# Kernel optimization log

Measured on AMD Instinct MI355X. Metric: run time of the kernel, lower is better.

The kernel has to match this reference:

```python
import jax, jax.numpy as jnp
import numpy as np

B, C, L = 4, 512, 4096
LN_EPS = 1e-5


def setup_inputs() -> dict:
    key = jax.random.key(0)
    ks = jax.random.split(key, 6)
    s = 1.0 / np.sqrt(C)
    return {
        "x": jax.random.normal(ks[0], (B, C, L), dtype=jnp.float32),
        "ln_w": jnp.ones((C,), dtype=jnp.float32),
        "ln_b": jnp.zeros((C,), dtype=jnp.float32),
        "wq": jax.random.normal(ks[1], (C, C), dtype=jnp.float32) * s,
        "bq": jnp.zeros((C,), dtype=jnp.float32),
        "wk": jax.random.normal(ks[2], (C, C), dtype=jnp.float32) * s,
        "bk": jnp.zeros((C,), dtype=jnp.float32),
        "wv": jax.random.normal(ks[3], (C, C), dtype=jnp.float32) * s,
        "bv": jnp.zeros((C,), dtype=jnp.float32),
        "wp": jax.random.normal(ks[4], (C, C), dtype=jnp.float32) * s,
        "bp": jnp.zeros((C,), dtype=jnp.float32),
    }


def reference(x, ln_w, ln_b, wq, bq, wk, bk, wv, bv, wp, bp):
    # x: [b, c, l]. LayerNorm over channels (permute -> LN -> permute back).
    xt = jnp.swapaxes(x, 1, 2)  # [b, l, c]
    mu = jnp.mean(xt, axis=-1, keepdims=True)
    var = jnp.var(xt, axis=-1, keepdims=True)
    h = (xt - mu) * jax.lax.rsqrt(var + LN_EPS) * ln_w + ln_b  # [b, l, c]

    # 1x1 convs == channel-mixing matmuls (weight [out, in])
    q = jnp.einsum('blc,oc->blo', h, wq) + bq  # [b, l, c]
    k = jnp.einsum('blc,oc->blo', h, wk) + bk
    v = jnp.einsum('blc,oc->blo', h, wv) + bv

    c = x.shape[1]
    scores = jnp.einsum('blc,bmc->blm', q, k) * (float(c) ** -0.5)  # [b, l_q, l_k]
    attn = jax.nn.softmax(scores, axis=-1)
    o = jnp.einsum('blm,bmc->blc', attn, v)  # [b, l, c]

    o = jnp.einsum('blc,oc->blo', o, wp) + bp
    o = jax.nn.selu(o)
    return x + jnp.swapaxes(o, 1, 2)  # [b, c, l]
```

## Files before the change

### kernel.cpp

```cpp
#include <hip/hip_runtime.h>


typedef __attribute__((ext_vector_type(8))) __bf16 bf16x8;
typedef __attribute__((ext_vector_type(4))) __bf16 bf16x4;
typedef __attribute__((ext_vector_type(4))) float  f32x4;

__device__ __forceinline__ f32x4 mfma16(bf16x8 a, bf16x8 b, f32x4 c) {
  return __builtin_amdgcn_mfma_f32_16x16x32_bf16(a, b, c, 0, 0, 0);
}

__device__ __forceinline__ void gll16(const void* g, void* l) {
  __builtin_amdgcn_global_load_lds(
      (const __attribute__((address_space(1))) unsigned int*)g,
      (__attribute__((address_space(3))) unsigned int*)l, 16, 0, 0);
}

__device__ __forceinline__ float selu_f(float v) {
  return 1.0507009873554805f * (v > 0.f ? v : 1.6732632423543772f * (__expf(v) - 1.f));
}

#define QSCALE ((float)(1.4426950408889634 / 22.627416997969522))

__global__ __launch_bounds__(256) void cvt_w(const float* __restrict__ w0,
                                             const float* __restrict__ w1,
                                             const float* __restrict__ w2,
                                             const float* __restrict__ w3,
                                             __bf16* __restrict__ dst) {
  int idx = blockIdx.x * 256 + threadIdx.x;
  int which = idx >> 16;
  const float* s = which == 0 ? w0 : which == 1 ? w1 : which == 2 ? w2 : w3;
  f32x4 v = *(const f32x4*)(s + (size_t)(idx & 65535) * 4);
  bf16x4 o = {(__bf16)v.x, (__bf16)v.y, (__bf16)v.z, (__bf16)v.w};
  *(bf16x4*)(dst + (size_t)idx * 4) = o;
}

__global__ __launch_bounds__(256) void ln_stats(const float* __restrict__ x,
                                                float* __restrict__ mu,
                                                float* __restrict__ rs) {
  __shared__ float shs[4][64], shq[4][64];
  int b = blockIdx.y, l0 = blockIdx.x * 64;
  int i = threadIdx.x & 63, j = threadIdx.x >> 6;
  const float* xp = x + (size_t)b * 512 * 4096 + l0 + i;
  float s = 0.f, sq = 0.f;
  for (int c = j; c < 512; c += 4) {
    float v = xp[(size_t)c * 4096];
    s += v; sq += v * v;
  }
  shs[j][i] = s; shq[j][i] = sq;
  __syncthreads();
  if (threadIdx.x < 64) {
    float S = shs[0][i] + shs[1][i] + shs[2][i] + shs[3][i];
    float Q = shq[0][i] + shq[1][i] + shq[2][i] + shq[3][i];
    float m = S * (1.f / 512.f);
    float var = Q * (1.f / 512.f) - m * m;
    int idx = b * 4096 + l0 + i;
    mu[idx] = m;
    rs[idx] = rsqrtf(var + 1e-5f);
  }
}

__global__ __launch_bounds__(256) void ln_apply(const float* __restrict__ x,
                                                const float* __restrict__ mu,
                                                const float* __restrict__ rs,
                                                const float* __restrict__ lw,
                                                const float* __restrict__ lb,
                                                __bf16* __restrict__ h) {
  __shared__ float t[64][65];
  int b = blockIdx.z, c0 = blockIdx.y * 64, l0 = blockIdx.x * 64;
  int li = threadIdx.x & 63, r4 = threadIdx.x >> 6;
  const float* xp = x + (size_t)(b * 512 + c0) * 4096 + l0;
#pragma unroll
  for (int rr = 0; rr < 16; ++rr) {
    int cl = rr * 4 + r4;
    t[cl][li] = xp[(size_t)cl * 4096 + li];
  }
  __syncthreads();
  float gw = lw[c0 + li], gb = lb[c0 + li];
#pragma unroll
  for (int rr = 0; rr < 16; ++rr) {
    int lr = rr * 4 + r4;
    int l = l0 + lr;
    float m = mu[b * 4096 + l], r = rs[b * 4096 + l];
    float v = (t[li][lr] - m) * r * gw + gb;
    h[((size_t)b * 4096 + l) * 512 + c0 + li] = (__bf16)v;
  }
}

__global__ __launch_bounds__(256, 2) void gemm_qkv(
    const __bf16* __restrict__ A, const __bf16* __restrict__ W,
    const float* __restrict__ b0, const float* __restrict__ b1,
    const float* __restrict__ b2, __bf16* __restrict__ out,
    __bf16* __restrict__ vt) {
  __shared__ __align__(16) __bf16 As[128 * 64];
  __shared__ __align__(16) __bf16 Bs[128 * 64];
  const int tid = threadIdx.x;
  const int w = tid >> 6, lane = tid & 63, g = lane >> 4, li = lane & 15;
  const int id = blockIdx.x;
  const int jj = id >> 3;
  const int m0 = (16 * (id & 7) + jj / 12) * 128;
  const int n0 = (jj % 12) * 128;
  const int wm = w >> 1, wn = w & 1;
  const int srow = lane >> 3;
  const int scol = ((lane & 7) ^ srow) * 8;
  f32x4 acc[4][4] = {};
  for (int kt = 0; kt < 8; ++kt) {
    __syncthreads();
#pragma unroll
    for (int qq = 0; qq < 4; ++qq) {
      int r = w * 32 + qq * 8;
      gll16(A + (size_t)(m0 + r + srow) * 512 + kt * 64 + scol, &As[r * 64]);
      gll16(W + (size_t)(n0 + r + srow) * 512 + kt * 64 + scol, &Bs[r * 64]);
    }
    __syncthreads();
#pragma unroll
    for (int kk = 0; kk < 2; ++kk) {
      bf16x8 af[4], bf[4];
#pragma unroll
      for (int t = 0; t < 4; ++t) {
        int ra = wm * 64 + t * 16 + li;
        af[t] = *(const bf16x8*)&As[ra * 64 + ((kk * 32 + 8 * g) ^ ((ra & 7) * 8))];
        int rb = wn * 64 + t * 16 + li;
        bf[t] = *(const bf16x8*)&Bs[rb * 64 + ((kk * 32 + 8 * g) ^ ((rb & 7) * 8))];
      }
#pragma unroll
      for (int i = 0; i < 4; ++i)
#pragma unroll
        for (int j = 0; j < 4; ++j) acc[i][j] = mfma16(af[i], bf[j], acc[i][j]);
    }
  }
  const int which = n0 >> 9;
  if (which < 2) {
    const float* bb = which == 0 ? b0 : b1;
    const float sc = which == 0 ? QSCALE : 1.0f;
    __bf16* o = out + (size_t)which * 8388608;
#pragma unroll
    for (int i = 0; i < 4; ++i) {
#pragma unroll
      for (int j = 0; j < 4; ++j) {
        int r = m0 + wm * 64 + i * 16 + 4 * g;
        int c = (n0 & 511) + wn * 64 + j * 16 + li;
        float bv = bb[c];
#pragma unroll
        for (int e = 0; e < 4; ++e)
          o[(size_t)(r + e) * 512 + c] = (__bf16)((acc[i][j][e] + bv) * sc);
      }
    }
  } else {
#pragma unroll
    for (int i = 0; i < 4; ++i) {
#pragma unroll
      for (int j = 0; j < 4; ++j) {
        int r = m0 + wm * 64 + i * 16 + 4 * g;
        int c = (n0 & 511) + wn * 64 + j * 16 + li;
        float bv = b2[c];
#pragma unroll
        for (int e = 0; e < 4; ++e) {
          int row = r + e;
          vt[((size_t)(row >> 12) * 512 + c) * 4096 + (row & 4095)] =
              (__bf16)(acc[i][j][e] + bv);
        }
      }
    }
  }
}

__global__ __launch_bounds__(256, 2) void gemm_pp(
    const __bf16* __restrict__ A, const __bf16* __restrict__ Bm,
    const float* __restrict__ bias, const float* __restrict__ xres,
    float* __restrict__ out) {
  __shared__ __align__(16) __bf16 As[128 * 64];
  __shared__ __align__(16) __bf16 Bs[128 * 64];
  const int tid = threadIdx.x;
  const int w = tid >> 6, lane = tid & 63, g = lane >> 4, li = lane & 15;
  const int id = blockIdx.x;
  const int jj = id >> 3;
  const int n0 = (16 * (id & 7) + (jj & 15)) * 128;
  const int m0 = (jj >> 4) * 128;
  const int wm = w >> 1, wn = w & 1;
  const int srow = lane >> 3;
  const int scol = ((lane & 7) ^ srow) * 8;
  f32x4 acc[4][4] = {};
  for (int kt = 0; kt < 8; ++kt) {
    __syncthreads();
#pragma unroll
    for (int qq = 0; qq < 4; ++qq) {
      int r = w * 32 + qq * 8;
      gll16(A + (size_t)(m0 + r + srow) * 512 + kt * 64 + scol, &As[r * 64]);
      gll16(Bm + (size_t)(n0 + r + srow) * 512 + kt * 64 + scol, &Bs[r * 64]);
    }
    __syncthreads();
#pragma unroll
    for (int kk = 0; kk < 2; ++kk) {
      bf16x8 af[4], bf[4];
#pragma unroll
      for (int t = 0; t < 4; ++t) {
        int ra = wm * 64 + t * 16 + li;
        af[t] = *(const bf16x8*)&As[ra * 64 + ((kk * 32 + 8 * g) ^ ((ra & 7) * 8))];
        int rb = wn * 64 + t * 16 + li;
        bf[t] = *(const bf16x8*)&Bs[rb * 64 + ((kk * 32 + 8 * g) ^ ((rb & 7) * 8))];
      }
#pragma unroll
      for (int i = 0; i < 4; ++i)
#pragma unroll
        for (int j = 0; j < 4; ++j) acc[i][j] = mfma16(af[i], bf[j], acc[i][j]);
    }
  }
#pragma unroll
  for (int i = 0; i < 4; ++i) {
#pragma unroll
    for (int j = 0; j < 4; ++j) {
      int r = m0 + wm * 64 + i * 16 + 4 * g;
      int c = n0 + wn * 64 + j * 16 + li;
      int bb = c >> 12, l = c & 4095;
#pragma unroll
      for (int e = 0; e < 4; ++e) {
        float v = acc[i][j][e] + bias[r + e];
        size_t oi = ((size_t)bb * 512 + (r + e)) * 4096 + l;
        out[oi] = xres[oi] + selu_f(v);
      }
    }
  }
}

__global__ __launch_bounds__(512, 2) void flash_half(
    const __bf16* __restrict__ Q, const __bf16* __restrict__ K,
    const __bf16* __restrict__ VT, __bf16* __restrict__ Op,
    float* __restrict__ stats) {
  __shared__ __align__(16) __bf16 Ks[64][512];
  __shared__ __align__(16) __bf16 VTs[512][64];
  __shared__ __align__(16) __bf16 Ps[128][64];

  const int tid = threadIdx.x;
  const int w = tid >> 6, lane = tid & 63, g = lane >> 4, li = lane & 15;
  const int id = blockIdx.x;
  const int grp = id & 7;
  const int b = grp >> 1, half = grp & 1;
  const int q0 = (id >> 3) * 128;
  const size_t base = (size_t)b * (4096 * 512);
  const int kvbase = half * 2048;

  bf16x8 qf[16];
  {
    const __bf16* qp = Q + base + (size_t)(q0 + 16 * w + li) * 512 + 8 * g;
#pragma unroll
    for (int ks = 0; ks < 16; ++ks) qf[ks] = *(const bf16x8*)(qp + ks * 32);
  }

  f32x4 acc[8][4] = {};
  f32x4 lacc = {};
  bf16x8 ones;
#pragma unroll
  for (int j = 0; j < 8; ++j) ones[j] = (__bf16)1.0f;

  auto stageK = [&](int kt) {
#pragma unroll
    for (int i = 0; i < 8; ++i) {
      int r = w * 8 + i;
      int y = (lane * 16) ^ ((r & 7) << 4);
      gll16(K + base + (size_t)(kvbase + kt * 64 + r) * 512 + (y >> 1),
            &Ks[r][0]);
    }
  };
  auto stageVT = [&](int kt) {
    const int drow = lane >> 3;
    const int gr = (lane & 7) ^ drow;
#pragma unroll
    for (int i = 0; i < 8; ++i) {
      int d0 = w * 64 + i * 8;
      gll16(VT + (size_t)b * 2097152 + (size_t)(d0 + drow) * 4096 +
                kvbase + kt * 64 + gr * 8,
            &VTs[d0][0]);
    }
  };

  stageK(0);
  stageVT(0);
  __syncthreads();

  for (int kt = 0; kt < 32; ++kt) {
    __builtin_amdgcn_s_setprio(1);
    f32x4 s[4] = {};
#pragma unroll
    for (int ks = 0; ks < 16; ++ks) {
      int e = (ks * 32 + 8 * g) ^ ((li & 7) * 8);
#pragma unroll
      for (int kvt = 0; kvt < 4; ++kvt) {
        bf16x8 kf = *(const bf16x8*)&Ks[kvt * 16 + li][e];
        s[kvt] = mfma16(qf[ks], kf, s[kvt]);
      }
    }
    __builtin_amdgcn_s_setprio(0);

#pragma unroll
    for (int kvt = 0; kvt < 4; ++kvt) {
#pragma unroll
      for (int e = 0; e < 4; ++e) {
        float p = exp2f(s[kvt][e]);
        int row = 16 * w + 4 * g + e;
        int slot = (2 * kvt + (li >> 3)) ^ (row & 7);
        Ps[row][slot * 8 + (li & 7)] = (__bf16)p;
      }
    }
    __syncthreads();

    if (kt + 1 < 32) stageK(kt + 1);

#pragma unroll
    for (int ks = 0; ks < 2; ++ks) {
      bf16x8 bfr[4];
#pragma unroll
      for (int ct = 0; ct < 4; ++ct) {
        int dcol = 64 * w + 16 * ct + li;
        int slot = (4 * ks + g) ^ (li & 7);
        bfr[ct] = *(const bf16x8*)&VTs[dcol][slot * 8];
      }
      __builtin_amdgcn_s_setprio(1);
#pragma unroll
      for (int rt = 0; rt < 8; ++rt) {
        int prow = rt * 16 + li;
        int slot = (4 * ks + g) ^ (li & 7);
        bf16x8 af = *(const bf16x8*)&Ps[prow][slot * 8];
        if (rt == w) lacc = mfma16(af, ones, lacc);
#pragma unroll
        for (int ct = 0; ct < 4; ++ct)
          acc[rt][ct] = mfma16(af, bfr[ct], acc[rt][ct]);
      }
      __builtin_amdgcn_s_setprio(0);
    }
    __syncthreads();

    if (kt + 1 < 32) stageVT(kt + 1);
  }

  if (li == 0)
    *(f32x4*)(stats + half * 16384 + b * 4096 + q0 + 16 * w + 4 * g) = lacc;
#pragma unroll
  for (int rt = 0; rt < 8; ++rt) {
#pragma unroll
    for (int ct = 0; ct < 4; ++ct) {
      int rr = q0 + rt * 16 + 4 * g;
      int cc = w * 64 + ct * 16 + li;
#pragma unroll
      for (int e = 0; e < 4; ++e)
        Op[(size_t)half * 8388608 + base + (size_t)(rr + e) * 512 + cc] =
            (__bf16)acc[rt][ct][e];
    }
  }
}

__global__ __launch_bounds__(256) void combine2(const __bf16* __restrict__ Op,
                                                const float* __restrict__ stats,
                                                __bf16* __restrict__ ao) {
  int gid = blockIdx.x * 256 + threadIdx.x;
  int row = gid >> 6;
  int c = (gid & 63) * 8;
  float l0 = stats[row], l1 = stats[16384 + row];
  float inv = 1.f / (l0 + l1);
  bf16x8 v0 = *(const bf16x8*)(Op + (size_t)row * 512 + c);
  bf16x8 v1 = *(const bf16x8*)(Op + 8388608 + (size_t)row * 512 + c);
  bf16x8 o;
#pragma unroll
  for (int j = 0; j < 8; ++j)
    o[j] = (__bf16)(((float)v0[j] + (float)v1[j]) * inv);
  *(bf16x8*)(ao + (size_t)row * 512 + c) = o;
}

extern "C" void kernel_launch(void* const* d_in, const int* in_sizes, int n_in,
                              void* d_out, int out_size, void* d_ws, size_t ws_size,
                              hipStream_t stream) {
  const float* x   = (const float*)d_in[0];
  const float* lnw = (const float*)d_in[1];
  const float* lnb = (const float*)d_in[2];
  const float* wq  = (const float*)d_in[3];
  const float* bq  = (const float*)d_in[4];
  const float* wk  = (const float*)d_in[5];
  const float* bk  = (const float*)d_in[6];
  const float* wv  = (const float*)d_in[7];
  const float* bv  = (const float*)d_in[8];
  const float* wp  = (const float*)d_in[9];
  const float* bp  = (const float*)d_in[10];

  char* ws = (char*)d_ws;
  const size_t MB = 1024 * 1024;
  __bf16* h    = (__bf16*)(ws);
  __bf16* q    = (__bf16*)(ws + 16 * MB);
  __bf16* vt   = (__bf16*)(ws + 48 * MB);
  __bf16* wbf  = (__bf16*)(ws + 64 * MB);
  float*  mu   = (float*)(ws + 66 * MB);
  float*  rsg  = (float*)(ws + 66 * MB + 65536);
  __bf16* op   = (__bf16*)(ws + 67 * MB);
  float*  stats= (float*)(ws + 99 * MB);
  __bf16* ao   = h;

  cvt_w<<<1024, 256, 0, stream>>>(wq, wk, wv, wp, wbf);
  ln_stats<<<dim3(64, 4), 256, 0, stream>>>(x, mu, rsg);
  ln_apply<<<dim3(64, 8, 4), 256, 0, stream>>>(x, mu, rsg, lnw, lnb, h);
  gemm_qkv<<<1536, 256, 0, stream>>>(h, wbf, bq, bk, bv, q, vt);
  flash_half<<<256, 512, 0, stream>>>(q, q + 8388608, vt, op, stats);
  combine2<<<4096, 256, 0, stream>>>(op, stats, ao);
  gemm_pp<<<512, 256, 0, stream>>>(wbf + 3 * 262144, ao, bp, x,
                                   (float*)d_out);
}
```

Before: 341.6 us.

## Split attention KV into four partitions with smaller KV tiles

Attention now splits the key/value range into four partitions instead of two, with 32-key tiles instead of 64. This doubles the block count so every CU gets work and shrinks shared memory per block. Partial outputs go into reused scratch buffers (the LayerNorm buffer, the output buffer, a new region), and a four-way combine normalizes them. The cost is more partial-output traffic, more synchronization per key processed, and a tighter launch bound that may force register spills.

```diff
diff --git a/kernel.cpp b/kernel.cpp
--- a/kernel.cpp
+++ b/kernel.cpp
@@ -222,22 +222,25 @@
   }
 }
 
-__global__ __launch_bounds__(512, 2) void flash_half(
+__global__ __launch_bounds__(512, 4) void flash_quarter(
     const __bf16* __restrict__ Q, const __bf16* __restrict__ K,
-    const __bf16* __restrict__ VT, __bf16* __restrict__ Op,
+    const __bf16* __restrict__ VT,
+    __bf16* __restrict__ o0, __bf16* __restrict__ o1,
+    __bf16* __restrict__ o2, __bf16* __restrict__ o3,
     float* __restrict__ stats) {
-  __shared__ __align__(16) __bf16 Ks[64][512];
-  __shared__ __align__(16) __bf16 VTs[512][64];
-  __shared__ __align__(16) __bf16 Ps[128][64];
+  __shared__ __align__(16) __bf16 Ks[32][512];
+  __shared__ __align__(16) __bf16 VTs[512][32];
+  __shared__ __align__(16) __bf16 Ps[128][32];
 
   const int tid = threadIdx.x;
   const int w = tid >> 6, lane = tid & 63, g = lane >> 4, li = lane & 15;
   const int id = blockIdx.x;
-  const int grp = id & 7;
-  const int b = grp >> 1, half = grp & 1;
-  const int q0 = (id >> 3) * 128;
+  const int grp = id & 15;
+  const int b = grp >> 2, quarter = grp & 3;
+  const int q0 = (id >> 4) * 128;
   const size_t base = (size_t)b * (4096 * 512);
-  const int kvbase = half * 2048;
+  const int kvbase = quarter * 1024;
+  __bf16* Op = quarter == 0 ? o0 : quarter == 1 ? o1 : quarter == 2 ? o2 : o3;
 
   bf16x8 qf[16];
   {
@@ -254,21 +257,21 @@
 
   auto stageK = [&](int kt) {
 #pragma unroll
-    for (int i = 0; i < 8; ++i) {
-      int r = w * 8 + i;
+    for (int i = 0; i < 4; ++i) {
+      int r = w * 4 + i;
       int y = (lane * 16) ^ ((r & 7) << 4);
-      gll16(K + base + (size_t)(kvbase + kt * 64 + r) * 512 + (y >> 1),
+      gll16(K + base + (size_t)(kvbase + kt * 32 + r) * 512 + (y >> 1),
             &Ks[r][0]);
     }
   };
   auto stageVT = [&](int kt) {
-    const int drow = lane >> 3;
-    const int gr = (lane & 7) ^ drow;
-#pragma unroll
-    for (int i = 0; i < 8; ++i) {
-      int d0 = w * 64 + i * 8;
+    const int drow = lane >> 2;
+    const int gr = (lane & 3) ^ (drow & 3);
+#pragma unroll
+    for (int i = 0; i < 4; ++i) {
+      int d0 = w * 64 + i * 16;
       gll16(VT + (size_t)b * 2097152 + (size_t)(d0 + drow) * 4096 +
-                kvbase + kt * 64 + gr * 8,
+                kvbase + kt * 32 + gr * 8,
             &VTs[d0][0]);
     }
   };
@@ -279,12 +282,12 @@
 
   for (int kt = 0; kt < 32; ++kt) {
     __builtin_amdgcn_s_setprio(1);
-    f32x4 s[4] = {};
+    f32x4 s[2] = {};
 #pragma unroll
     for (int ks = 0; ks < 16; ++ks) {
       int e = (ks * 32 + 8 * g) ^ ((li & 7) * 8);
 #pragma unroll
-      for (int kvt = 0; kvt < 4; ++kvt) {
+      for (int kvt = 0; kvt < 2; ++kvt) {
         bf16x8 kf = *(const bf16x8*)&Ks[kvt * 16 + li][e];
         s[kvt] = mfma16(qf[ks], kf, s[kvt]);
       }
@@ -292,77 +295,77 @@
     __builtin_amdgcn_s_setprio(0);
 
 #pragma unroll
-    for (int kvt = 0; kvt < 4; ++kvt) {
+    for (int kvt = 0; kvt < 2; ++kvt) {
 #pragma unroll
       for (int e = 0; e < 4; ++e) {
         float p = exp2f(s[kvt][e]);
-        int row = 16 * w + 4 * g + e;
-        int slot = (2 * kvt + (li >> 3)) ^ (row & 7);
-        Ps[row][slot * 8 + (li & 7)] = (__bf16)p;
+        int slot = (2 * kvt + (li >> 3)) ^ (e & 3) ^ g;
+        Ps[16 * w + 4 * g + e][slot * 8 + (li & 7)] = (__bf16)p;
       }
     }
     __syncthreads();
 
     if (kt + 1 < 32) stageK(kt + 1);
 
-#pragma unroll
-    for (int ks = 0; ks < 2; ++ks) {
-      bf16x8 bfr[4];
-#pragma unroll
-      for (int ct = 0; ct < 4; ++ct) {
-        int dcol = 64 * w + 16 * ct + li;
-        int slot = (4 * ks + g) ^ (li & 7);
-        bfr[ct] = *(const bf16x8*)&VTs[dcol][slot * 8];
-      }
-      __builtin_amdgcn_s_setprio(1);
-#pragma unroll
-      for (int rt = 0; rt < 8; ++rt) {
-        int prow = rt * 16 + li;
-        int slot = (4 * ks + g) ^ (li & 7);
-        bf16x8 af = *(const bf16x8*)&Ps[prow][slot * 8];
-        if (rt == w) lacc = mfma16(af, ones, lacc);
-#pragma unroll
-        for (int ct = 0; ct < 4; ++ct)
-          acc[rt][ct] = mfma16(af, bfr[ct], acc[rt][ct]);
-      }
-      __builtin_amdgcn_s_setprio(0);
-    }
+    bf16x8 bfr[4];
+#pragma unroll
+    for (int ct = 0; ct < 4; ++ct) {
+      int dcol = 64 * w + ct * 16 + li;
+      int slot = g ^ (dcol & 3);
+      bfr[ct] = *(const bf16x8*)&VTs[dcol][slot * 8];
+    }
+    __builtin_amdgcn_s_setprio(1);
+#pragma unroll
+    for (int rt = 0; rt < 8; ++rt) {
+      int prow = rt * 16 + li;
+      int slot = g ^ (li & 3) ^ ((li >> 2) & 3);
+      bf16x8 af = *(const bf16x8*)&Ps[prow][slot * 8];
+      if (rt == w) lacc = mfma16(af, ones, lacc);
+#pragma unroll
+      for (int ct = 0; ct < 4; ++ct)
+        acc[rt][ct] = mfma16(af, bfr[ct], acc[rt][ct]);
+    }
+    __builtin_amdgcn_s_setprio(0);
     __syncthreads();
 
     if (kt + 1 < 32) stageVT(kt + 1);
   }
 
   if (li == 0)
-    *(f32x4*)(stats + half * 16384 + b * 4096 + q0 + 16 * w + 4 * g) = lacc;
+    *(f32x4*)(stats + quarter * 16384 + b * 4096 + q0 + 16 * w + 4 * g) = lacc;
 #pragma unroll
   for (int rt = 0; rt < 8; ++rt) {
 #pragma unroll
     for (int ct = 0; ct < 4; ++ct) {
       int rr = q0 + rt * 16 + 4 * g;
-      int cc = w * 64 + ct * 16 + li;
+      int cc = 64 * w + ct * 16 + li;
 #pragma unroll
       for (int e = 0; e < 4; ++e)
-        Op[(size_t)half * 8388608 + base + (size_t)(rr + e) * 512 + cc] =
-            (__bf16)acc[rt][ct][e];
-    }
-  }
-}
-
-__global__ __launch_bounds__(256) void combine2(const __bf16* __restrict__ Op,
-                                                const float* __restrict__ stats,
-                                                __bf16* __restrict__ ao) {
+        Op[base + (size_t)(rr + e) * 512 + cc] = (__bf16)acc[rt][ct][e];
+    }
+  }
+}
+
+__global__ __launch_bounds__(256) void combine4(
+    const __bf16* __restrict__ o0, const __bf16* __restrict__ o1,
+    const __bf16* __restrict__ o2, const __bf16* __restrict__ o3,
+    const float* __restrict__ stats, __bf16* __restrict__ ao) {
   int gid = blockIdx.x * 256 + threadIdx.x;
   int row = gid >> 6;
   int c = (gid & 63) * 8;
-  float l0 = stats[row], l1 = stats[16384 + row];
-  float inv = 1.f / (l0 + l1);
-  bf16x8 v0 = *(const bf16x8*)(Op + (size_t)row * 512 + c);
-  bf16x8 v1 = *(const bf16x8*)(Op + 8388608 + (size_t)row * 512 + c);
+  float l = stats[row] + stats[16384 + row] + stats[32768 + row] +
+            stats[49152 + row];
+  float inv = 1.f / l;
+  size_t off = (size_t)row * 512 + c;
+  bf16x8 v0 = *(const bf16x8*)(o0 + off);
+  bf16x8 v1 = *(const bf16x8*)(o1 + off);
+  bf16x8 v2 = *(const bf16x8*)(o2 + off);
+  bf16x8 v3 = *(const bf16x8*)(o3 + off);
   bf16x8 o;
 #pragma unroll
   for (int j = 0; j < 8; ++j)
-    o[j] = (__bf16)(((float)v0[j] + (float)v1[j]) * inv);
-  *(bf16x8*)(ao + (size_t)row * 512 + c) = o;
+    o[j] = (__bf16)(((float)v0[j] + (float)v1[j] + (float)v2[j] + (float)v3[j]) * inv);
+  *(bf16x8*)(ao + off) = o;
 }
 
 extern "C" void kernel_launch(void* const* d_in, const int* in_sizes, int n_in,
@@ -388,16 +391,20 @@
   __bf16* wbf  = (__bf16*)(ws + 64 * MB);
   float*  mu   = (float*)(ws + 66 * MB);
   float*  rsg  = (float*)(ws + 66 * MB + 65536);
-  __bf16* op   = (__bf16*)(ws + 67 * MB);
-  float*  stats= (float*)(ws + 99 * MB);
-  __bf16* ao   = h;
+  __bf16* op3  = (__bf16*)(ws + 67 * MB);
+  float*  stats= (float*)(ws + 83 * MB);
+  __bf16* op0  = h;
+  __bf16* op1  = (__bf16*)d_out;
+  __bf16* op2  = (__bf16*)d_out + 8388608;
+  __bf16* ao   = vt;
 
   cvt_w<<<1024, 256, 0, stream>>>(wq, wk, wv, wp, wbf);
   ln_stats<<<dim3(64, 4), 256, 0, stream>>>(x, mu, rsg);
   ln_apply<<<dim3(64, 8, 4), 256, 0, stream>>>(x, mu, rsg, lnw, lnb, h);
   gemm_qkv<<<1536, 256, 0, stream>>>(h, wbf, bq, bk, bv, q, vt);
-  flash_half<<<256, 512, 0, stream>>>(q, q + 8388608, vt, op, stats);
-  combine2<<<4096, 256, 0, stream>>>(op, stats, ao);
+  flash_quarter<<<512, 512, 0, stream>>>(q, q + 8388608, vt,
+                                         op0, op1, op2, op3, stats);
+  combine4<<<4096, 256, 0, stream>>>(op0, op1, op2, op3, stats, ao);
   gemm_pp<<<512, 256, 0, stream>>>(wbf + 3 * 262144, ao, bp, x,
                                    (float*)d_out);
 }
```

After: 1.152 ms. +237.2%, slower.
